# Optimization experiments

Measured on AMD Instinct MI355X. Metric: run time of the kernel, lower is better.

The kernel has to match this reference:

```python
import jax, jax.numpy as jnp
import numpy as np

N = 50000      # nodes
E = 800000     # edges
FEAT = 128     # input feature dim
EMB = 256      # embed_dim = heads * hid
H = 4          # attention heads
C = 64         # hid_dim per head
PED = 32       # positional encoding dim
NEG_SLOPE = 0.2


def setup_inputs() -> dict:
    key = jax.random.key(0)
    ks = jax.random.split(key, 20)
    s = lambda i, shape, sc=0.1: jax.random.normal(ks[i], shape, jnp.float32) * sc
    return {
        "x": s(0, (N, FEAT), 1.0),
        "x_masked": s(1, (N, FEAT), 1.0),
        "PE": s(2, (N, PED), 1.0),
        "PE_noise": s(3, (N, PED), 1.0),
        "edge_index": jax.random.randint(ks[4], (2, E), 0, N),
        # PEG positional encoder (linear + relu)
        "W_peg": s(5, (PED, PED)), "b_peg": jnp.zeros((PED,), jnp.float32),
        # GAT layer 0
        "W0": s(6, (FEAT, H * C)), "a_s0": s(7, (H, C)), "a_d0": s(8, (H, C)),
        "w_pe0": s(9, (H,)), "W_u0": s(10, (PED, PED)),
        # GAT layer 1
        "W1": s(11, (EMB, H * C)), "a_s1": s(12, (H, C)), "a_d1": s(13, (H, C)),
        "w_pe1": s(14, (H,)), "W_u1": s(15, (PED, PED)),
    }


def _gat(x, pe, src, dst, W, a_s, a_d, w_pe, W_u):
    # PE-aware GATConv: standard GAT attention + PE-distance bias per head.
    xp = (x @ W).reshape(-1, H, C)                       # [N,H,C]
    al_s = (xp * a_s).sum(-1)                            # [N,H]
    al_d = (xp * a_d).sum(-1)                            # [N,H]
    dist = jnp.sqrt(((pe[src] - pe[dst]) ** 2).sum(-1) + 1e-8)   # [E]
    logits = jax.nn.leaky_relu(al_s[src] + al_d[dst], NEG_SLOPE) \
             + dist[:, None] * w_pe                      # [E,H]
    # segment softmax over incoming edges of each dst node
    m = jax.ops.segment_max(logits, dst, num_segments=N)
    e = jnp.exp(logits - m[dst])
    den = jax.ops.segment_sum(e, dst, num_segments=N)
    alpha = e / (den[dst] + 1e-16)                       # [E,H]
    out = jax.ops.segment_sum(alpha[:, :, None] * xp[src], dst,
                              num_segments=N).reshape(-1, H * C)  # [N,H*C]
    pe_out = jax.nn.relu(pe @ W_u)                       # per-layer PE update
    return out, pe_out


def reference(x, x_masked, PE, PE_noise, W_peg, b_peg,
              W0, a_s0, a_d0, w_pe0, W_u0,
              W1, a_s1, a_d1, w_pe1, W_u1, edge_index):
    src, dst = edge_index[0], edge_index[1]
    # PEG encoder on both PE branches
    pe = jax.nn.relu(PE @ W_peg + b_peg)
    pe_n = jax.nn.relu(PE_noise @ W_peg + b_peg)
    # layer 0 (dual branches; eval mode -> dropout is identity)
    h, pe_n = _gat(x, pe_n, src, dst, W0, a_s0, a_d0, w_pe0, W_u0)
    hm, pe = _gat(x_masked, pe, src, dst, W0, a_s0, a_d0, w_pe0, W_u0)
    h = jax.nn.relu(h)
    hm = jax.nn.relu(hm)
    # layer 1 (last layer: no activation)
    h, pe_n = _gat(h, pe_n, src, dst, W1, a_s1, a_d1, w_pe1, W_u1)
    hm, pe = _gat(hm, pe, src, dst, W1, a_s1, a_d1, w_pe1, W_u1)
    return (hm, pe_n)
```

## Files before the change

### kernel.cpp

```cpp
#include <hip/hip_runtime.h>
#include <hip/hip_bf16.h>

#define N_NODES 50000
#define N_EDGES 800000
#define NEG_SLOPE 0.2f

typedef __hip_bfloat16 bf16;
typedef __attribute__((ext_vector_type(8))) short short8;
typedef __attribute__((ext_vector_type(4))) float f32x4;

__device__ __forceinline__ float b2f(bf16 x) { return __bfloat162float(x); }

__device__ __forceinline__ float ldsel(const void* p, size_t i, int isbf) {
  return isbf ? __bfloat162float(((const bf16*)p)[i]) : ((const float*)p)[i];
}
__device__ __forceinline__ void stsel(void* p, size_t i, int isbf, float v) {
  if (isbf) ((bf16*)p)[i] = __float2bfloat16(v);
  else ((float*)p)[i] = v;
}

__device__ __forceinline__ int block_detect(const unsigned short* __restrict__ probe) {
  __shared__ int wcount;
  int tid = threadIdx.x;
  if (tid == 0) wcount = 0;
  __syncthreads();
  int ex = (probe[2 * tid] >> 7) & 0xFF;
  unsigned long long m = __ballot(ex >= 0x85);
  if ((tid & 63) == 0) atomicAdd(&wcount, __popcll(m));
  __syncthreads();
  return wcount < 8;
}

struct CvtJobs {
  const void* src[10];
  float* dst[10];
  int n[10];
};
__global__ __launch_bounds__(256) void prep_kernel(CvtJobs jobs,
                                                   const unsigned short* __restrict__ probe,
                                                   const void* __restrict__ W0in,
                                                   bf16* __restrict__ Wt0,
                                                   const void* __restrict__ W1in,
                                                   bf16* __restrict__ Wt1,
                                                   int* __restrict__ flag) {
  int tid = threadIdx.x;
  int isbf = block_detect(probe);
  int b = blockIdx.x;
  if (b == 0 && tid == 0) *flag = isbf;
  if (b < 16) {
    for (int j = 0; j < 10; j++) {
      int n = jobs.n[j];
      const void* s = jobs.src[j];
      float* d = jobs.dst[j];
      for (int i = b * 256 + tid; i < n; i += 16 * 256) d[i] = ldsel(s, i, isbf);
    }
  } else if (b < 16 + 128) {
    int i = (b - 16) * 256 + tid;
    int n = i >> 7, k = i & 127;
    Wt0[i] = __float2bfloat16(ldsel(W0in, (size_t)k * 256 + n, isbf));
  } else {
    int i = (b - 144) * 256 + tid;
    int n = i >> 8, k = i & 255;
    Wt1[i] = __float2bfloat16(ldsel(W1in, (size_t)k * 256 + n, isbf));
  }
}

__global__ __launch_bounds__(256) void peg_all(const void* __restrict__ pen,
                                               const void* __restrict__ pem,
                                               const float* __restrict__ Wpeg,
                                               const float* __restrict__ bpeg,
                                               const float* __restrict__ Wu0,
                                               const float* __restrict__ Wu1,
                                               void* out, size_t out_off,
                                               bf16* __restrict__ pe0,
                                               bf16* __restrict__ pe1,
                                               const int* __restrict__ flag) {
  __shared__ float w1[1024], w2[1024], w3[1024];
  __shared__ float rowA[256], rowB[256];
  int isbf = *flag;
  int tid = threadIdx.x;
  int b = blockIdx.x;
  bool c3 = b < (N_NODES / 8);
  int n0 = (c3 ? b : b - N_NODES / 8) * 8;
  const void* in = c3 ? pen : pem;
  for (int i = tid; i < 1024; i += 256) {
    w1[i] = Wpeg[i];
    w2[i] = Wu0[i];
    if (c3) w3[i] = Wu1[i];
  }
  rowA[tid] = ldsel(in, (size_t)n0 * 32 + tid, isbf);
  __syncthreads();
  int col = tid & 31, ln = tid >> 5;
  float acc = bpeg[col];
#pragma unroll
  for (int j = 0; j < 32; j++) acc += rowA[ln * 32 + j] * w1[j * 32 + col];
  acc = fmaxf(acc, 0.f);
  if (!c3) pe0[(size_t)n0 * 32 + tid] = __float2bfloat16(acc);
  rowB[tid] = acc;
  __syncthreads();
  acc = 0.f;
#pragma unroll
  for (int j = 0; j < 32; j++) acc += rowB[ln * 32 + j] * w2[j * 32 + col];
  acc = fmaxf(acc, 0.f);
  if (!c3) {
    pe1[(size_t)n0 * 32 + tid] = __float2bfloat16(acc);
    return;
  }
  rowA[tid] = acc;
  __syncthreads();
  acc = 0.f;
#pragma unroll
  for (int j = 0; j < 32; j++) acc += rowA[ln * 32 + j] * w3[j * 32 + col];
  stsel(out, out_off + (size_t)n0 * 32 + tid, isbf, fmaxf(acc, 0.f));
}

template <int K, bool A_DUAL>
__global__ __launch_bounds__(256) void mfma_gemm(const void* __restrict__ Ap,
                                                 const bf16* __restrict__ Bt,
                                                 bf16* __restrict__ C, int M,
                                                 const float* __restrict__ a_sf,
                                                 const float* __restrict__ a_df,
                                                 float* __restrict__ al_s,
                                                 float* __restrict__ al_d,
                                                 const int* __restrict__ flag) {
  constexpr int LDK = 136;
  __shared__ short a_lds[64 * LDK];
  __shared__ short b_lds[64 * LDK];
  __shared__ float lds_al[128];
  int nrt = (M + 63) / 64;
  int bid = blockIdx.x;
  int xcd = bid & 7;
  int jj = bid >> 3;
  int col_t = jj & 3;
  int row_t = (jj >> 2) * 8 + xcd;
  if (row_t >= nrt) return;
  int isbf = A_DUAL ? *flag : 1;
  int tid = threadIdx.x;
  int row0 = row_t * 64;
  int col0 = col_t * 64;
  int lane = tid & 63;
  int wv = tid >> 6;
  int wm = (wv & 1) * 32, wn = (wv >> 1) * 32;
  int l15 = lane & 15, quad = lane >> 4;
  if (tid < 128) lds_al[tid] = 0.f;
  f32x4 acc00 = {0.f, 0.f, 0.f, 0.f}, acc01 = acc00, acc10 = acc00, acc11 = acc00;

  for (int kb = 0; kb < K; kb += 128) {
    if (kb) __syncthreads();
    for (int idx = tid; idx < 64 * 16; idx += 256) {
      int r = idx >> 4, sidx = idx & 15;
      int gr = row0 + r;
      size_t gi = (size_t)gr * K + kb + sidx * 8;
      uint4 av = make_uint4(0u, 0u, 0u, 0u);
      if (A_DUAL && !isbf) {
        if (gr < M) {
          float4 f0 = ((const float4*)Ap)[gi / 4];
          float4 f1 = ((const float4*)Ap)[gi / 4 + 1];
          union { uint4 v; bf16 h[8]; } o;
          o.h[0] = __float2bfloat16(f0.x);
          o.h[1] = __float2bfloat16(f0.y);
          o.h[2] = __float2bfloat16(f0.z);
          o.h[3] = __float2bfloat16(f0.w);
          o.h[4] = __float2bfloat16(f1.x);
          o.h[5] = __float2bfloat16(f1.y);
          o.h[6] = __float2bfloat16(f1.z);
          o.h[7] = __float2bfloat16(f1.w);
          av = o.v;
        }
      } else {
        if (gr < M) av = *(const uint4*)&((const bf16*)Ap)[gi];
      }
      *(uint4*)&a_lds[r * LDK + sidx * 8] = av;
      *(uint4*)&b_lds[r * LDK + sidx * 8] =
          *(const uint4*)&Bt[(size_t)(col0 + r) * K + kb + sidx * 8];
    }
    __syncthreads();
#pragma unroll
    for (int k0 = 0; k0 < 128; k0 += 32) {
      int ko = k0 + quad * 8;
      short8 a0 = *(const short8*)&a_lds[(wm + l15) * LDK + ko];
      short8 a1 = *(const short8*)&a_lds[(wm + 16 + l15) * LDK + ko];
      short8 b0 = *(const short8*)&b_lds[(wn + l15) * LDK + ko];
      short8 b1 = *(const short8*)&b_lds[(wn + 16 + l15) * LDK + ko];
      acc00 = __builtin_amdgcn_mfma_f32_16x16x32_bf16(a0, b0, acc00, 0, 0, 0);
      acc01 = __builtin_amdgcn_mfma_f32_16x16x32_bf16(a0, b1, acc01, 0, 0, 0);
      acc10 = __builtin_amdgcn_mfma_f32_16x16x32_bf16(a1, b0, acc10, 0, 0, 0);
      acc11 = __builtin_amdgcn_mfma_f32_16x16x32_bf16(a1, b1, acc11, 0, 0, 0);
    }
  }
  const f32x4* accs[2][2] = {{&acc00, &acc01}, {&acc10, &acc11}};
  float as0 = a_sf[col0 + wn + l15], as1 = a_sf[col0 + wn + 16 + l15];
  float ad0 = a_df[col0 + wn + l15], ad1 = a_df[col0 + wn + 16 + l15];
#pragma unroll
  for (int i = 0; i < 2; i++) {
    float sp[4], dp[4];
#pragma unroll
    for (int r = 0; r < 4; r++) {
      float v0 = (*accs[i][0])[r], v1 = (*accs[i][1])[r];
      sp[r] = v0 * as0 + v1 * as1;
      dp[r] = v0 * ad0 + v1 * ad1;
      int grow = row0 + wm + i * 16 + quad * 4 + r;
      if (grow < M) {
        C[(size_t)grow * 256 + col0 + wn + l15] = __float2bfloat16(v0);
        C[(size_t)grow * 256 + col0 + wn + 16 + l15] = __float2bfloat16(v1);
      }
    }
#pragma unroll
    for (int off = 1; off < 16; off <<= 1) {
#pragma unroll
      for (int r = 0; r < 4; r++) {
        sp[r] += __shfl_xor(sp[r], off);
        dp[r] += __shfl_xor(dp[r], off);
      }
    }
    if (l15 == 0) {
#pragma unroll
      for (int r = 0; r < 4; r++) {
        int lrow = wm + i * 16 + quad * 4 + r;
        atomicAdd(&lds_al[lrow], sp[r]);
        atomicAdd(&lds_al[64 + lrow], dp[r]);
      }
    }
  }
  __syncthreads();
  if (tid < 64 && row0 + tid < M) {
    al_s[(size_t)(row0 + tid) * 4 + col_t] = lds_al[tid];
    al_d[(size_t)(row0 + tid) * 4 + col_t] = lds_al[64 + tid];
  }
}

__global__ __launch_bounds__(256) void hist_kernel(const int* __restrict__ dst,
                                                   int* __restrict__ deg) {
  int e = blockIdx.x * 256 + threadIdx.x;
  atomicAdd(&deg[dst[e]], 1);
}

__global__ __launch_bounds__(1024) void scan1_kernel(const int* __restrict__ deg,
                                                     int* __restrict__ tmp,
                                                     int* __restrict__ bsum, int n) {
  __shared__ int wsum[16];
  int tid = threadIdx.x;
  int idx = blockIdx.x * 1024 + tid;
  int v = (idx < n) ? deg[idx] : 0;
  int incl = v;
#pragma unroll
  for (int off = 1; off < 64; off <<= 1) {
    int t = __shfl_up(incl, off);
    if ((tid & 63) >= off) incl += t;
  }
  int wid = tid >> 6;
  if ((tid & 63) == 63) wsum[wid] = incl;
  __syncthreads();
  if (tid == 0) {
    int acc = 0;
#pragma unroll
    for (int w = 0; w < 16; w++) {
      int t = wsum[w];
      wsum[w] = acc;
      acc += t;
    }
    bsum[blockIdx.x] = acc;
  }
  __syncthreads();
  if (idx < n) tmp[idx] = wsum[wid] + incl;
}

__global__ void scan2_kernel(int* __restrict__ bsum, int nb) {
  int tid = threadIdx.x;
  int v = (tid < nb) ? bsum[tid] : 0;
  int incl = v;
#pragma unroll
  for (int off = 1; off < 64; off <<= 1) {
    int t = __shfl_up(incl, off);
    if (tid >= off) incl += t;
  }
  if (tid < nb) bsum[tid] = incl - v;
}

__global__ __launch_bounds__(1024) void scan3_kernel(const int* __restrict__ tmp,
                                                     const int* __restrict__ bsum,
                                                     int* __restrict__ rowptr, int n) {
  int idx = blockIdx.x * 1024 + threadIdx.x;
  if (idx < n) rowptr[idx + 1] = tmp[idx] + bsum[blockIdx.x];
  if (idx == 0) rowptr[0] = 0;
}

__global__ __launch_bounds__(256) void fill_kernel(const int* __restrict__ src,
                                                   const int* __restrict__ dst,
                                                   const int* __restrict__ rowptr,
                                                   int* __restrict__ fill,
                                                   int* __restrict__ csr_src) {
  int e = blockIdx.x * 256 + threadIdx.x;
  int d = dst[e];
  int pos = atomicAdd(&fill[d], 1);
  csr_src[rowptr[d] + pos] = src[e];
}

template <bool RELU, bool OUT_DUAL>
__global__ __launch_bounds__(256) void agg_kernel(const bf16* __restrict__ xp,
                                                  const bf16* __restrict__ pe,
                                                  const float* __restrict__ al_s,
                                                  const float* __restrict__ al_d,
                                                  const float* __restrict__ w_pe,
                                                  const int* __restrict__ csr_src,
                                                  const int* __restrict__ rowptr,
                                                  void* out, const int* __restrict__ flag) {
  int isbf = OUT_DUAL ? *flag : 1;
  int lane = threadIdx.x & 63;
  int n = blockIdx.x * 4 + (threadIdx.x >> 6);
  int q = lane >> 4, li = lane & 15, h = li >> 2;
  unsigned int ud = *(const unsigned int*)&pe[(size_t)n * 32 + li * 2];
  float pdlo = __uint_as_float(ud << 16);
  float pdhi = __uint_as_float(ud & 0xffff0000u);
  float ald = al_d[(size_t)n * 4 + h];
  float wph = w_pe[h];
  int rp = rowptr[n], s1 = rowptr[n + 1];
  int niter = (s1 - rp + 7) >> 3;
  int s = rp + q;
  float acc[16];
#pragma unroll
  for (int j = 0; j < 16; j++) acc[j] = 0.f;
  float asum = 0.f;

  auto LD = [&](int sn, unsigned int& pes, float& als, uint4& x0, uint4& x1) {
    int idx = sn >= 0 ? sn : 0;
    pes = *(const unsigned int*)&pe[(size_t)idx * 32 + li * 2];
    float a = al_s[(size_t)idx * 4 + h];
    als = sn >= 0 ? a : -1e30f;
    const uint4* b = (const uint4*)&xp[(size_t)idx * 256 + li * 16];
    x0 = b[0];
    x1 = b[1];
  };
  auto COMPUTE = [&](unsigned int pes, float als, uint4 v0, uint4 v1) {
    float dx = __uint_as_float(pes << 16) - pdlo;
    float dy = __uint_as_float(pes & 0xffff0000u) - pdhi;
    float d2 = dx * dx + dy * dy;
#pragma unroll
    for (int off = 1; off < 16; off <<= 1) d2 += __shfl_xor(d2, off);
    float lg = als + ald;
    lg = (lg >= 0.f) ? lg : NEG_SLOPE * lg;
    lg += sqrtf(d2 + 1e-8f) * wph;
    float a = __expf(lg);
    unsigned int u[8] = {v0.x, v0.y, v0.z, v0.w, v1.x, v1.y, v1.z, v1.w};
#pragma unroll
    for (int p = 0; p < 8; p++) {
      acc[2 * p] += a * __uint_as_float(u[p] << 16);
      acc[2 * p + 1] += a * __uint_as_float(u[p] & 0xffff0000u);
    }
    asum += a;
  };

  int sc0 = -1, sc1 = -1, sn0 = -1, sn1 = -1;
  unsigned int pc0 = 0, pc1 = 0, pn0 = 0, pn1 = 0;
  float ac0 = -1e30f, ac1 = -1e30f, an0 = -1e30f, an1 = -1e30f;
  uint4 z = make_uint4(0u, 0u, 0u, 0u);
  uint4 xc00 = z, xc01 = z, xc10 = z, xc11 = z;
  uint4 xn00 = z, xn01 = z, xn10 = z, xn11 = z;

  if (niter > 0) {
    sc0 = (s < s1) ? csr_src[s] : -1;
    sc1 = (s + 4 < s1) ? csr_src[s + 4] : -1;
    LD(sc0, pc0, ac0, xc00, xc01);
    LD(sc1, pc1, ac1, xc10, xc11);
    sn0 = (s + 8 < s1) ? csr_src[s + 8] : -1;
    sn1 = (s + 12 < s1) ? csr_src[s + 12] : -1;
  }
  for (int t = 0; t < niter; t++) {
    LD(sn0, pn0, an0, xn00, xn01);
    LD(sn1, pn1, an1, xn10, xn11);
    int sb = s + 8 * t + 16;
    int sf0 = (sb < s1) ? csr_src[sb] : -1;
    int sf1 = (sb + 4 < s1) ? csr_src[sb + 4] : -1;
    COMPUTE(pc0, ac0, xc00, xc01);
    COMPUTE(pc1, ac1, xc10, xc11);
    sc0 = sn0; sc1 = sn1;
    pc0 = pn0; pc1 = pn1;
    ac0 = an0; ac1 = an1;
    xc00 = xn00; xc01 = xn01; xc10 = xn10; xc11 = xn11;
    sn0 = sf0; sn1 = sf1;
  }
#pragma unroll
  for (int j = 0; j < 16; j++) {
    acc[j] += __shfl_xor(acc[j], 16);
    acc[j] += __shfl_xor(acc[j], 32);
  }
  asum += __shfl_xor(asum, 16);
  asum += __shfl_xor(asum, 32);
  if (q == 0) {
    float inv = 1.f / (asum + 1e-16f);
    size_t oi = (size_t)n * 256 + li * 16;
    if (OUT_DUAL && !isbf) {
      float* of = (float*)out;
#pragma unroll
      for (int p = 0; p < 4; p++) {
        float4 f;
        f.x = acc[4 * p] * inv;
        f.y = acc[4 * p + 1] * inv;
        f.z = acc[4 * p + 2] * inv;
        f.w = acc[4 * p + 3] * inv;
        if (RELU) {
          f.x = fmaxf(f.x, 0.f);
          f.y = fmaxf(f.y, 0.f);
          f.z = fmaxf(f.z, 0.f);
          f.w = fmaxf(f.w, 0.f);
        }
        *(float4*)&of[oi + 4 * p] = f;
      }
    } else {
      union { uint4 v[2]; bf16 hh[16]; } o;
#pragma unroll
      for (int j = 0; j < 16; j++) {
        float r = acc[j] * inv;
        if (RELU) r = fmaxf(r, 0.f);
        o.hh[j] = __float2bfloat16(r);
      }
      uint4* ob = (uint4*)&((bf16*)out)[oi];
      ob[0] = o.v[0];
      ob[1] = o.v[1];
    }
  }
}

extern "C" void kernel_launch(void* const* d_in, const int* in_sizes, int n_in,
                              void* d_out, int out_size, void* d_ws, size_t ws_size,
                              hipStream_t stream) {
  const void* x_masked = d_in[1];
  const void* PE = d_in[2];
  const void* PE_noise = d_in[3];
  const int* ei = (const int*)d_in[4];
  const int* src = ei;
  const int* dst = ei + N_EDGES;

  char* w = (char*)d_ws;
  auto alloc = [&](size_t bytes) -> char* {
    char* p = w;
    w += (bytes + 255) / 256 * 256;
    return p;
  };
  int* flag = (int*)alloc(4);
  float* W_peg_f = (float*)alloc(1024 * 4);
  float* b_peg_f = (float*)alloc(32 * 4);
  float* a_s0_f = (float*)alloc(256 * 4);
  float* a_d0_f = (float*)alloc(256 * 4);
  float* w_pe0_f = (float*)alloc(4 * 4);
  float* W_u0_f = (float*)alloc(1024 * 4);
  float* a_s1_f = (float*)alloc(256 * 4);
  float* a_d1_f = (float*)alloc(256 * 4);
  float* w_pe1_f = (float*)alloc(4 * 4);
  float* W_u1_f = (float*)alloc(1024 * 4);
  bf16* Wt0 = (bf16*)alloc(32768 * 2);
  bf16* Wt1 = (bf16*)alloc(65536 * 2);
  bf16* pe0_bf = (bf16*)alloc((size_t)N_NODES * 32 * 2);
  bf16* pe1_bf = (bf16*)alloc((size_t)N_NODES * 32 * 2);
  float* al_s = (float*)alloc((size_t)N_NODES * 4 * 4);
  float* al_d = (float*)alloc((size_t)N_NODES * 4 * 4);
  int* degfill = (int*)alloc((size_t)N_NODES * 2 * 4);
  int* deg = degfill;
  int* fill = degfill + N_NODES;
  int* rowptr = (int*)alloc((size_t)(N_NODES + 1) * 4);
  int* stmp = (int*)alloc((size_t)N_NODES * 4);
  int* bsum = (int*)alloc(64 * 4);
  int* csr_src = (int*)alloc((size_t)N_EDGES * 4);
  bf16* xp = (bf16*)alloc((size_t)N_NODES * 256 * 2);
  bf16* hm0 = (bf16*)alloc((size_t)N_NODES * 256 * 2);

  CvtJobs jobs;
  int ji = 0;
  auto addjob = [&](const void* s, float* d, int n) {
    jobs.src[ji] = s; jobs.dst[ji] = d; jobs.n[ji] = n; ji++;
  };
  addjob(d_in[5], W_peg_f, 1024);
  addjob(d_in[6], b_peg_f, 32);
  addjob(d_in[8], a_s0_f, 256);
  addjob(d_in[9], a_d0_f, 256);
  addjob(d_in[10], w_pe0_f, 4);
  addjob(d_in[11], W_u0_f, 1024);
  addjob(d_in[13], a_s1_f, 256);
  addjob(d_in[14], a_d1_f, 256);
  addjob(d_in[15], w_pe1_f, 4);
  addjob(d_in[16], W_u1_f, 1024);
  prep_kernel<<<400, 256, 0, stream>>>(jobs, (const unsigned short*)d_in[5],
                                       d_in[7], Wt0, d_in[12], Wt1, flag);

  hipMemsetAsync(degfill, 0, (size_t)N_NODES * 2 * 4, stream);

  hist_kernel<<<N_EDGES / 256, 256, 0, stream>>>(dst, deg);
  scan1_kernel<<<49, 1024, 0, stream>>>(deg, stmp, bsum, N_NODES);
  scan2_kernel<<<1, 64, 0, stream>>>(bsum, 49);
  scan3_kernel<<<49, 1024, 0, stream>>>(stmp, bsum, rowptr, N_NODES);
  fill_kernel<<<N_EDGES / 256, 256, 0, stream>>>(src, dst, rowptr, fill, csr_src);

  peg_all<<<2 * (N_NODES / 8), 256, 0, stream>>>(PE_noise, PE, W_peg_f, b_peg_f,
                                                 W_u0_f, W_u1_f, d_out,
                                                 (size_t)N_NODES * 256, pe0_bf,
                                                 pe1_bf, flag);

  int nrt = (N_NODES + 63) / 64;
  int gblk = ((nrt + 7) / 8) * 8 * 4;

  mfma_gemm<128, true><<<gblk, 256, 0, stream>>>(x_masked, Wt0, xp, N_NODES,
                                                 a_s0_f, a_d0_f, al_s, al_d, flag);
  agg_kernel<true, false><<<N_NODES / 4, 256, 0, stream>>>(
      xp, pe0_bf, al_s, al_d, w_pe0_f, csr_src, rowptr, hm0, flag);

  mfma_gemm<256, false><<<gblk, 256, 0, stream>>>(hm0, Wt1, xp, N_NODES,
                                                  a_s1_f, a_d1_f, al_s, al_d, flag);
  agg_kernel<false, true><<<N_NODES / 4, 256, 0, stream>>>(
      xp, pe1_bf, al_s, al_d, w_pe1_f, csr_src, rowptr, d_out, flag);
}
```

Measured before the change: 458.3 us.

## Interleave PE and al_s per node into one blob; simplify agg gather pipeline

The per-node positional encoding (bf16, 64 B) and the source attention scalars al_s (4 floats) now live together in one 128-byte record per node. Each gathered edge therefore touches a single cache line instead of two scattered arrays. The aggregation loop drops the two-edges-per-iteration scheme for a single-edge software pipeline with a prefetched next index, uses packed float2 accumulators, and switches to a fast sqrt and a branchless leaky ReLU. The blob wastes about 60 bytes of padding per node, and the shallower prefetch depth may expose more gather latency.

```diff
diff --git a/kernel.cpp b/kernel.cpp
--- a/kernel.cpp
+++ b/kernel.cpp
@@ -8,6 +8,7 @@
 typedef __hip_bfloat16 bf16;
 typedef __attribute__((ext_vector_type(8))) short short8;
 typedef __attribute__((ext_vector_type(4))) float f32x4;
+typedef __attribute__((ext_vector_type(2))) float f32x2;
 
 __device__ __forceinline__ float b2f(bf16 x) { return __bfloat162float(x); }
 
@@ -72,8 +73,8 @@
                                                const float* __restrict__ Wu0,
                                                const float* __restrict__ Wu1,
                                                void* out, size_t out_off,
-                                               bf16* __restrict__ pe0,
-                                               bf16* __restrict__ pe1,
+                                               char* __restrict__ blob0,
+                                               char* __restrict__ blob1,
                                                const int* __restrict__ flag) {
   __shared__ float w1[1024], w2[1024], w3[1024];
   __shared__ float rowA[256], rowB[256];
@@ -91,11 +92,12 @@
   rowA[tid] = ldsel(in, (size_t)n0 * 32 + tid, isbf);
   __syncthreads();
   int col = tid & 31, ln = tid >> 5;
+  size_t bi = ((size_t)(n0 + ln)) * 64 + col;
   float acc = bpeg[col];
 #pragma unroll
   for (int j = 0; j < 32; j++) acc += rowA[ln * 32 + j] * w1[j * 32 + col];
   acc = fmaxf(acc, 0.f);
-  if (!c3) pe0[(size_t)n0 * 32 + tid] = __float2bfloat16(acc);
+  if (!c3) ((bf16*)blob0)[bi] = __float2bfloat16(acc);
   rowB[tid] = acc;
   __syncthreads();
   acc = 0.f;
@@ -103,7 +105,7 @@
   for (int j = 0; j < 32; j++) acc += rowB[ln * 32 + j] * w2[j * 32 + col];
   acc = fmaxf(acc, 0.f);
   if (!c3) {
-    pe1[(size_t)n0 * 32 + tid] = __float2bfloat16(acc);
+    ((bf16*)blob1)[bi] = __float2bfloat16(acc);
     return;
   }
   rowA[tid] = acc;
@@ -120,7 +122,7 @@
                                                  bf16* __restrict__ C, int M,
                                                  const float* __restrict__ a_sf,
                                                  const float* __restrict__ a_df,
-                                                 float* __restrict__ al_s,
+                                                 char* __restrict__ blob,
                                                  float* __restrict__ al_d,
                                                  const int* __restrict__ flag) {
   constexpr int LDK = 136;
@@ -224,8 +226,9 @@
   }
   __syncthreads();
   if (tid < 64 && row0 + tid < M) {
-    al_s[(size_t)(row0 + tid) * 4 + col_t] = lds_al[tid];
-    al_d[(size_t)(row0 + tid) * 4 + col_t] = lds_al[64 + tid];
+    int row = row0 + tid;
+    *(float*)(blob + (size_t)row * 128 + 64 + (size_t)col_t * 4) = lds_al[tid];
+    al_d[(size_t)row * 4 + col_t] = lds_al[64 + tid];
   }
 }
 
@@ -298,8 +301,7 @@
 
 template <bool RELU, bool OUT_DUAL>
 __global__ __launch_bounds__(256) void agg_kernel(const bf16* __restrict__ xp,
-                                                  const bf16* __restrict__ pe,
-                                                  const float* __restrict__ al_s,
+                                                  const char* __restrict__ blob,
                                                   const float* __restrict__ al_d,
                                                   const float* __restrict__ w_pe,
                                                   const int* __restrict__ csr_src,
@@ -309,80 +311,78 @@
   int lane = threadIdx.x & 63;
   int n = blockIdx.x * 4 + (threadIdx.x >> 6);
   int q = lane >> 4, li = lane & 15, h = li >> 2;
-  unsigned int ud = *(const unsigned int*)&pe[(size_t)n * 32 + li * 2];
+  const char* bn = blob + (size_t)n * 128;
+  unsigned int ud = *(const unsigned int*)(bn + li * 4);
   float pdlo = __uint_as_float(ud << 16);
   float pdhi = __uint_as_float(ud & 0xffff0000u);
   float ald = al_d[(size_t)n * 4 + h];
   float wph = w_pe[h];
-  int rp = rowptr[n], s1 = rowptr[n + 1];
-  int niter = (s1 - rp + 7) >> 3;
-  int s = rp + q;
-  float acc[16];
-#pragma unroll
-  for (int j = 0; j < 16; j++) acc[j] = 0.f;
+  int s1 = rowptr[n + 1];
+  int s = rowptr[n] + q;
+  f32x2 acc2[8];
+#pragma unroll
+  for (int j = 0; j < 8; j++) acc2[j] = (f32x2){0.f, 0.f};
   float asum = 0.f;
 
-  auto LD = [&](int sn, unsigned int& pes, float& als, uint4& x0, uint4& x1) {
-    int idx = sn >= 0 ? sn : 0;
-    pes = *(const unsigned int*)&pe[(size_t)idx * 32 + li * 2];
-    float a = al_s[(size_t)idx * 4 + h];
-    als = sn >= 0 ? a : -1e30f;
-    const uint4* b = (const uint4*)&xp[(size_t)idx * 256 + li * 16];
-    x0 = b[0];
-    x1 = b[1];
-  };
-  auto COMPUTE = [&](unsigned int pes, float als, uint4 v0, uint4 v1) {
-    float dx = __uint_as_float(pes << 16) - pdlo;
-    float dy = __uint_as_float(pes & 0xffff0000u) - pdhi;
+  int sn_c = -1, sn_n = -1;
+  unsigned int pes_c = 0, pes_n = 0;
+  float als_c = 0.f, als_n = 0.f;
+  uint4 z = make_uint4(0u, 0u, 0u, 0u);
+  uint4 xc0 = z, xc1 = z, xn0 = z, xn1 = z;
+  if (s < s1) {
+    sn_c = csr_src[s];
+    const char* bs = blob + (size_t)sn_c * 128;
+    pes_c = *(const unsigned int*)(bs + li * 4);
+    als_c = *(const float*)(bs + 64 + h * 4);
+    const uint4* b = (const uint4*)&xp[(size_t)sn_c * 256 + li * 16];
+    xc0 = b[0];
+    xc1 = b[1];
+    if (s + 4 < s1) sn_n = csr_src[s + 4];
+  }
+  int sf = s + 8;
+  while (sn_c >= 0) {
+    if (sn_n >= 0) {
+      const char* bs = blob + (size_t)sn_n * 128;
+      pes_n = *(const unsigned int*)(bs + li * 4);
+      als_n = *(const float*)(bs + 64 + h * 4);
+      const uint4* b = (const uint4*)&xp[(size_t)sn_n * 256 + li * 16];
+      xn0 = b[0];
+      xn1 = b[1];
+    }
+    int sn_f = (sf < s1) ? csr_src[sf] : -1;
+    sf += 4;
+    float dx = __uint_as_float(pes_c << 16) - pdlo;
+    float dy = __uint_as_float(pes_c & 0xffff0000u) - pdhi;
     float d2 = dx * dx + dy * dy;
 #pragma unroll
     for (int off = 1; off < 16; off <<= 1) d2 += __shfl_xor(d2, off);
-    float lg = als + ald;
-    lg = (lg >= 0.f) ? lg : NEG_SLOPE * lg;
-    lg += sqrtf(d2 + 1e-8f) * wph;
+    float lg = als_c + ald;
+    lg = fmaxf(lg, 0.f) + NEG_SLOPE * fminf(lg, 0.f);
+    lg += __builtin_amdgcn_sqrtf(d2 + 1e-8f) * wph;
     float a = __expf(lg);
-    unsigned int u[8] = {v0.x, v0.y, v0.z, v0.w, v1.x, v1.y, v1.z, v1.w};
+    f32x2 av = {a, a};
+    unsigned int u[8] = {xc0.x, xc0.y, xc0.z, xc0.w, xc1.x, xc1.y, xc1.z, xc1.w};
 #pragma unroll
     for (int p = 0; p < 8; p++) {
-      acc[2 * p] += a * __uint_as_float(u[p] << 16);
-      acc[2 * p + 1] += a * __uint_as_float(u[p] & 0xffff0000u);
+      f32x2 xv;
+      xv.x = __uint_as_float(u[p] << 16);
+      xv.y = __uint_as_float(u[p] & 0xffff0000u);
+      acc2[p] += av * xv;
     }
     asum += a;
-  };
-
-  int sc0 = -1, sc1 = -1, sn0 = -1, sn1 = -1;
-  unsigned int pc0 = 0, pc1 = 0, pn0 = 0, pn1 = 0;
-  float ac0 = -1e30f, ac1 = -1e30f, an0 = -1e30f, an1 = -1e30f;
-  uint4 z = make_uint4(0u, 0u, 0u, 0u);
-  uint4 xc00 = z, xc01 = z, xc10 = z, xc11 = z;
-  uint4 xn00 = z, xn01 = z, xn10 = z, xn11 = z;
-
-  if (niter > 0) {
-    sc0 = (s < s1) ? csr_src[s] : -1;
-    sc1 = (s + 4 < s1) ? csr_src[s + 4] : -1;
-    LD(sc0, pc0, ac0, xc00, xc01);
-    LD(sc1, pc1, ac1, xc10, xc11);
-    sn0 = (s + 8 < s1) ? csr_src[s + 8] : -1;
-    sn1 = (s + 12 < s1) ? csr_src[s + 12] : -1;
-  }
-  for (int t = 0; t < niter; t++) {
-    LD(sn0, pn0, an0, xn00, xn01);
-    LD(sn1, pn1, an1, xn10, xn11);
-    int sb = s + 8 * t + 16;
-    int sf0 = (sb < s1) ? csr_src[sb] : -1;
-    int sf1 = (sb + 4 < s1) ? csr_src[sb + 4] : -1;
-    COMPUTE(pc0, ac0, xc00, xc01);
-    COMPUTE(pc1, ac1, xc10, xc11);
-    sc0 = sn0; sc1 = sn1;
-    pc0 = pn0; pc1 = pn1;
-    ac0 = an0; ac1 = an1;
-    xc00 = xn00; xc01 = xn01; xc10 = xn10; xc11 = xn11;
-    sn0 = sf0; sn1 = sf1;
-  }
-#pragma unroll
-  for (int j = 0; j < 16; j++) {
-    acc[j] += __shfl_xor(acc[j], 16);
-    acc[j] += __shfl_xor(acc[j], 32);
+    sn_c = sn_n;
+    pes_c = pes_n;
+    als_c = als_n;
+    xc0 = xn0;
+    xc1 = xn1;
+    sn_n = sn_f;
+  }
+#pragma unroll
+  for (int j = 0; j < 8; j++) {
+    acc2[j].x += __shfl_xor(acc2[j].x, 16);
+    acc2[j].x += __shfl_xor(acc2[j].x, 32);
+    acc2[j].y += __shfl_xor(acc2[j].y, 16);
+    acc2[j].y += __shfl_xor(acc2[j].y, 32);
   }
   asum += __shfl_xor(asum, 16);
   asum += __shfl_xor(asum, 32);
@@ -394,10 +394,10 @@
 #pragma unroll
       for (int p = 0; p < 4; p++) {
         float4 f;
-        f.x = acc[4 * p] * inv;
-        f.y = acc[4 * p + 1] * inv;
-        f.z = acc[4 * p + 2] * inv;
-        f.w = acc[4 * p + 3] * inv;
+        f.x = acc2[2 * p].x * inv;
+        f.y = acc2[2 * p].y * inv;
+        f.z = acc2[2 * p + 1].x * inv;
+        f.w = acc2[2 * p + 1].y * inv;
         if (RELU) {
           f.x = fmaxf(f.x, 0.f);
           f.y = fmaxf(f.y, 0.f);
@@ -409,10 +409,15 @@
     } else {
       union { uint4 v[2]; bf16 hh[16]; } o;
 #pragma unroll
-      for (int j = 0; j < 16; j++) {
-        float r = acc[j] * inv;
-        if (RELU) r = fmaxf(r, 0.f);
-        o.hh[j] = __float2bfloat16(r);
+      for (int j = 0; j < 8; j++) {
+        float rlo = acc2[j].x * inv;
+        float rhi = acc2[j].y * inv;
+        if (RELU) {
+          rlo = fmaxf(rlo, 0.f);
+          rhi = fmaxf(rhi, 0.f);
+        }
+        o.hh[2 * j] = __float2bfloat16(rlo);
+        o.hh[2 * j + 1] = __float2bfloat16(rhi);
       }
       uint4* ob = (uint4*)&((bf16*)out)[oi];
       ob[0] = o.v[0];
@@ -450,9 +455,8 @@
   float* W_u1_f = (float*)alloc(1024 * 4);
   bf16* Wt0 = (bf16*)alloc(32768 * 2);
   bf16* Wt1 = (bf16*)alloc(65536 * 2);
-  bf16* pe0_bf = (bf16*)alloc((size_t)N_NODES * 32 * 2);
-  bf16* pe1_bf = (bf16*)alloc((size_t)N_NODES * 32 * 2);
-  float* al_s = (float*)alloc((size_t)N_NODES * 4 * 4);
+  char* blob0 = alloc((size_t)N_NODES * 128);
+  char* blob1 = alloc((size_t)N_NODES * 128);
   float* al_d = (float*)alloc((size_t)N_NODES * 4 * 4);
   int* degfill = (int*)alloc((size_t)N_NODES * 2 * 4);
   int* deg = degfill;
@@ -492,19 +496,19 @@
 
   peg_all<<<2 * (N_NODES / 8), 256, 0, stream>>>(PE_noise, PE, W_peg_f, b_peg_f,
                                                  W_u0_f, W_u1_f, d_out,
-                                                 (size_t)N_NODES * 256, pe0_bf,
-                                                 pe1_bf, flag);
+                                                 (size_t)N_NODES * 256, blob0,
+                                                 blob1, flag);
 
   int nrt = (N_NODES + 63) / 64;
   int gblk = ((nrt + 7) / 8) * 8 * 4;
 
   mfma_gemm<128, true><<<gblk, 256, 0, stream>>>(x_masked, Wt0, xp, N_NODES,
-                                                 a_s0_f, a_d0_f, al_s, al_d, flag);
+                                                 a_s0_f, a_d0_f, blob0, al_d, flag);
   agg_kernel<true, false><<<N_NODES / 4, 256, 0, stream>>>(
-      xp, pe0_bf, al_s, al_d, w_pe0_f, csr_src, rowptr, hm0, flag);
+      xp, blob0, al_d, w_pe0_f, csr_src, rowptr, hm0, flag);
 
   mfma_gemm<256, false><<<gblk, 256, 0, stream>>>(hm0, Wt1, xp, N_NODES,
-                                                  a_s1_f, a_d1_f, al_s, al_d, flag);
+                                                  a_s1_f, a_d1_f, blob1, al_d, flag);
   agg_kernel<false, true><<<N_NODES / 4, 256, 0, stream>>>(
-      xp, pe1_bf, al_s, al_d, w_pe1_f, csr_src, rowptr, d_out, flag);
-}
+      xp, blob1, al_d, w_pe1_f, csr_src, rowptr, d_out, flag);
+}
```

After: 442.0 us. 3.5% less time.
